# Kernel tuning notes

Measured on AMD Instinct MI355X. Metric: run time of the kernel, lower is better.

Reference implementation:

```python
import jax, jax.numpy as jnp
import numpy as np

N_NODES = 100000
N_EDGES = 3200000
N_GRAPHS = 64
NEG_SLOPE = 0.2


def mish(x):
    return x * jnp.tanh(jax.nn.softplus(x))


def gat_layer(x, src, dst, W, b, a_src, a_dst, heads, out_ch, n_nodes):
    # h: [N, H, C]
    h = (x @ W).reshape(n_nodes, heads, out_ch)
    alpha_s = jnp.sum(h * a_src[None], axis=-1)  # [N, H]
    alpha_d = jnp.sum(h * a_dst[None], axis=-1)  # [N, H]
    e = jax.nn.leaky_relu(alpha_s[src] + alpha_d[dst], NEG_SLOPE)  # [E, H]
    # scatter-softmax over incoming edges of each destination node
    emax = jax.ops.segment_max(e, dst, num_segments=n_nodes)  # [N, H]
    ee = jnp.exp(e - emax[dst])
    den = jax.ops.segment_sum(ee, dst, num_segments=n_nodes)
    alpha = ee / (den[dst] + 1e-16)  # [E, H]
    msg = h[src] * alpha[..., None]  # [E, H, C]
    out = jax.ops.segment_sum(msg, dst, num_segments=n_nodes)
    return out.reshape(n_nodes, heads * out_ch) + b


def setup_inputs() -> dict:
    key = jax.random.key(0)
    ks = jax.random.split(key, 10)
    x = jax.random.normal(ks[0], (N_NODES, 128), dtype=jnp.float32)
    edge_index = jax.random.randint(ks[1], (2, N_EDGES), 0, N_NODES, dtype=jnp.int64)
    batch = jnp.sort(jax.random.randint(ks[2], (N_NODES,), 0, N_GRAPHS, dtype=jnp.int64))
    s1 = 1.0 / np.sqrt(128.0)
    s2 = 1.0 / np.sqrt(16.0)
    return {
        "x": x,
        "edge_index": edge_index,
        "batch": batch,
        "W1": jax.random.normal(ks[3], (128, 16), dtype=jnp.float32) * s1,
        "b1": jnp.zeros((16,), dtype=jnp.float32),
        "a_src1": jax.random.normal(ks[4], (4, 4), dtype=jnp.float32) * 0.5,
        "a_dst1": jax.random.normal(ks[5], (4, 4), dtype=jnp.float32) * 0.5,
        "W2": jax.random.normal(ks[6], (16, 32), dtype=jnp.float32) * s2,
        "b2": jnp.zeros((32,), dtype=jnp.float32),
        "a_src2": jax.random.normal(ks[7], (1, 32), dtype=jnp.float32) * 0.5,
        "a_dst2": jax.random.normal(ks[8], (1, 32), dtype=jnp.float32) * 0.5,
    }


def reference(x, edge_index, batch, W1, b1, a_src1, a_dst1, W2, b2, a_src2, a_dst2):
    n = x.shape[0]
    # PyG GATConv default add_self_loops=True
    loop = jnp.arange(n, dtype=edge_index.dtype)
    src = jnp.concatenate([edge_index[0], loop])
    dst = jnp.concatenate([edge_index[1], loop])
    h = mish(gat_layer(x, src, dst, W1, b1, a_src1, a_dst1, heads=4, out_ch=4, n_nodes=n))
    h = mish(gat_layer(h, src, dst, W2, b2, a_src2, a_dst2, heads=1, out_ch=32, n_nodes=n))
    # global_mean_pool
    sums = jax.ops.segment_sum(h, batch, num_segments=N_GRAPHS)
    cnts = jax.ops.segment_sum(jnp.ones((n,), h.dtype), batch, num_segments=N_GRAPHS)
    return sums / jnp.maximum(cnts, 1.0)[:, None]
```

## Files before the change

### kernel.cpp

```cpp
#include <hip/hip_runtime.h>
#include <hip/hip_fp16.h>
#include <math.h>

#define NEG_SLOPE 0.2f
#define SB 256
#define NBMAX 1024
#define CAP 5120

typedef _Float16 half2v __attribute__((ext_vector_type(2)));

__device__ __forceinline__ float mishf(float x) {
    if (x > 15.f) return x;
    float ex = __expf(x);
    float y = 1.f + ex;
    float y2 = y * y;
    return x * (y2 - 1.f) / (y2 + 1.f);
}

__device__ __forceinline__ float lw(float e) {
    return __expf(fmaxf(e, NEG_SLOPE * e));
}

__device__ __forceinline__ float hdot2(half2v a, half2v b) {
#if __has_builtin(__builtin_amdgcn_fdot2)
    return __builtin_amdgcn_fdot2(a, b, 0.f, false);
#else
    return (float)a.x * (float)b.x + (float)a.y * (float)b.y;
#endif
}

__global__ void gemm1_kernel(const float* __restrict__ x, const float* __restrict__ W1,
                             const float* __restrict__ a_dst,
                             const float* __restrict__ W2, const float* __restrict__ as2,
                             const float* __restrict__ ad2,
                             _Float16* __restrict__ hpre1h, float* __restrict__ addst,
                             int* __restrict__ cursor, float* __restrict__ pool,
                             float* __restrict__ cnt, float* __restrict__ vs,
                             float* __restrict__ vd, int NB, int NG, int N) {
    __shared__ float Wl[128 * 16];
    __shared__ float xs[16 * 132];
    int tid = threadIdx.x;
    if (blockIdx.x == 0) {
        for (int i = tid; i < NB; i += 256) cursor[i] = 0;
        for (int i = tid; i < NG * 32; i += 256) pool[i] = 0.f;
        for (int i = tid; i < NG; i += 256) cnt[i] = 0.f;
        if (tid < 16) {
            float ps = 0.f, pd = 0.f;
            #pragma unroll
            for (int c = 0; c < 32; c++) {
                float w = W2[tid * 32 + c];
                ps += w * as2[c];
                pd += w * ad2[c];
            }
            vs[tid] = ps; vd[tid] = pd;
        }
    }
    for (int i = tid; i < 2048; i += 256) Wl[i] = W1[i];
    int nodebase = blockIdx.x * 16;
    const float4* x4 = (const float4*)(x + (size_t)nodebase * 128);
    for (int i = tid; i < 512; i += 256) {
        float4 v = x4[i];
        int e = i * 4;
        int nl = e >> 7, k = e & 127;
        float* dp = &xs[nl * 132 + k];
        dp[0] = v.x; dp[1] = v.y; dp[2] = v.z; dp[3] = v.w;
    }
    __syncthreads();
    int nl = tid >> 4, ch = tid & 15;
    const float* xr = &xs[nl * 132];
    float acc = 0.f;
    #pragma unroll 8
    for (int k = 0; k < 128; k++) acc += xr[k] * Wl[k * 16 + ch];
    int node = nodebase + nl;
    if (node < N) {
        hpre1h[node * 16 + ch] = (_Float16)acc;
        float pd = acc * a_dst[ch];
        pd += __shfl_xor(pd, 1); pd += __shfl_xor(pd, 2);
        if ((ch & 3) == 0) addst[node * 4 + (ch >> 2)] = pd;
    }
}

__global__ __launch_bounds__(1024) void scatF_kernel(
        const int* __restrict__ src, const int* __restrict__ dst,
        int E, int Etot, int CH, int NB,
        int* __restrict__ cursor, int* __restrict__ pairs) {
    __shared__ int lcnt[NBMAX];
    __shared__ int lbase[NBMAX];
    int tid = threadIdx.x, blk = blockIdx.x;
    for (int b = tid; b < NB; b += 1024) lcnt[b] = 0;
    __syncthreads();
    int ibeg = blk * CH, iend = min((blk + 1) * CH, Etot);
    for (int i = ibeg + tid; i < iend; i += 1024) {
        int d = (i < E) ? dst[i] : (i - E);
        atomicAdd(&lcnt[d >> 7], 1);
    }
    __syncthreads();
    for (int b = tid; b < NB; b += 1024) {
        int h = lcnt[b];
        lbase[b] = h ? atomicAdd(&cursor[b], h) : 0;
    }
    __syncthreads();
    for (int b = tid; b < NB; b += 1024) lcnt[b] = 0;
    __syncthreads();
    for (int i = ibeg + tid; i < iend; i += 1024) {
        int s, d;
        if (i < E) { s = src[i]; d = dst[i]; } else { s = d = i - E; }
        int b = d >> 7, dl = d & 127;
        int r = atomicAdd(&lcnt[b], 1);
        int pos = lbase[b] + r;
        pairs[(size_t)b * CAP + (pos < CAP ? pos : CAP - 1)] = s | (dl << 17);
    }
}

__global__ __launch_bounds__(512) void csragg1_kernel(
        const int* __restrict__ pairs, const int* __restrict__ btotal,
        int NB, int N,
        int* __restrict__ ssorted, int* __restrict__ rs, int* __restrict__ re,
        const float* __restrict__ a_src1, const float* __restrict__ addst,
        const _Float16* __restrict__ hpre1h, const float* __restrict__ b1,
        const float* __restrict__ vs, const float* __restrict__ vd,
        _Float16* __restrict__ hpost1h,
        float* __restrict__ as2n, float* __restrict__ ad2n) {
    __shared__ int deg[128];
    __shared__ int s[128];
    __shared__ int cur[128];
    __shared__ __attribute__((aligned(16))) int lds_sorted[CAP];
    int tid = threadIdx.x, b = blockIdx.x;
    int nb0 = b << 7;
    int cnt_nodes = min(128, N - nb0);
    int bstart = b * CAP;
    int total = min(btotal[b], CAP);
    int bend = bstart + total;
    if (tid < 128) deg[tid] = 0;
    __syncthreads();
    for (int j = bstart + tid; j < bend; j += 512)
        atomicAdd(&deg[(pairs[j] >> 17) & 127], 1);
    __syncthreads();
    if (tid < 128) s[tid] = deg[tid];
    __syncthreads();
    for (int o = 1; o < 128; o <<= 1) {
        int v = 0;
        if (tid < 128 && tid >= o) v = s[tid - o];
        __syncthreads();
        if (tid < 128) s[tid] += v;
        __syncthreads();
    }
    if (tid < 128) {
        int ex = s[tid] - deg[tid];
        cur[tid] = ex;
        if (tid < cnt_nodes) {
            rs[nb0 + tid] = bstart + ex;
            re[nb0 + tid] = bstart + ex + deg[tid];
        }
    }
    __syncthreads();
    for (int j = bstart + tid; j < bend; j += 512) {
        int p = pairs[j];
        int pos = atomicAdd(&cur[(p >> 17) & 127], 1);
        lds_sorted[pos] = p & 0x1FFFF;
    }
    __syncthreads();

    {
        int t4 = total >> 2;
        const int4* ls4 = (const int4*)lds_sorted;
        int4* gs4 = (int4*)(ssorted + bstart);
        for (int j = tid; j < t4; j += 512) gs4[j] = ls4[j];
        for (int j = (t4 << 2) + tid; j < total; j += 512)
            ssorted[bstart + j] = lds_sorted[j];
    }

    int wave = tid >> 6;
    int lane = tid & 63;
    int er = lane >> 3, hc = lane & 7, head = hc >> 1;
    int c0 = hc * 2;
    half2v wsh;
    wsh.x = (_Float16)a_src1[c0];
    wsh.y = (_Float16)a_src1[c0 + 1];
    const _Float16* hb = hpre1h + c0;
    for (int r = 0; r < 16; r++) {
        int ln = (wave << 4) + r;
        if (ln >= cnt_nodes) break;
        int node = nb0 + ln;
        int end = cur[ln];
        int start = end - deg[ln];
        float adh = addst[node * 4 + head];
        float den = 0.f, a0 = 0.f, a1 = 0.f;
        int last = end - 1;
        int jb = start;
        for (; jb + 16 <= end; jb += 16) {
            int j0 = jb + er, j1 = j0 + 8;
            int s0 = lds_sorted[j0];
            int s1 = lds_sorted[j1];
            half2v h0 = *(const half2v*)(hb + s0 * 16);
            half2v h1 = *(const half2v*)(hb + s1 * 16);
            float p0 = hdot2(h0, wsh);
            float p1 = hdot2(h1, wsh);
            float w0 = lw(p0 + __shfl_xor(p0, 1) + adh);
            float w1 = lw(p1 + __shfl_xor(p1, 1) + adh);
            den += w0 + w1;
            a0 += (float)h0.x * w0 + (float)h1.x * w1;
            a1 += (float)h0.y * w0 + (float)h1.y * w1;
        }
        if (jb < end) {
            int j0 = jb + er, j1 = j0 + 8;
            int k0 = (j0 <= last) ? j0 : last;
            int k1 = (j1 <= last) ? j1 : last;
            int s0 = lds_sorted[k0];
            int s1 = lds_sorted[k1];
            half2v h0 = *(const half2v*)(hb + s0 * 16);
            half2v h1 = *(const half2v*)(hb + s1 * 16);
            float p0 = hdot2(h0, wsh);
            float p1 = hdot2(h1, wsh);
            float e0 = p0 + __shfl_xor(p0, 1) + adh;
            float e1 = p1 + __shfl_xor(p1, 1) + adh;
            float w0 = (j0 <= last) ? lw(e0) : 0.f;
            float w1 = (j1 <= last) ? lw(e1) : 0.f;
            den += w0 + w1;
            a0 += (float)h0.x * w0 + (float)h1.x * w1;
            a1 += (float)h0.y * w0 + (float)h1.y * w1;
        }
        a0 += __shfl_xor(a0, 8);  a1 += __shfl_xor(a1, 8);  den += __shfl_xor(den, 8);
        a0 += __shfl_xor(a0, 16); a1 += __shfl_xor(a1, 16); den += __shfl_xor(den, 16);
        a0 += __shfl_xor(a0, 32); a1 += __shfl_xor(a1, 32); den += __shfl_xor(den, 32);
        if (er == 0) {
            float inv = 1.f / (den + 1e-16f);
            float o0 = mishf(a0 * inv + b1[c0]);
            float o1 = mishf(a1 * inv + b1[c0 + 1]);
            half2v oh;
            oh.x = (_Float16)o0; oh.y = (_Float16)o1;
            *(half2v*)(hpost1h + node * 16 + c0) = oh;
            float ps = o0 * vs[c0] + o1 * vs[c0 + 1];
            float pd = o0 * vd[c0] + o1 * vd[c0 + 1];
            ps += __shfl_xor(ps, 1); pd += __shfl_xor(pd, 1);
            ps += __shfl_xor(ps, 2); pd += __shfl_xor(pd, 2);
            ps += __shfl_xor(ps, 4); pd += __shfl_xor(pd, 4);
            if (hc == 0) { as2n[node] = ps; ad2n[node] = pd; }
        }
    }
}

__global__ void agg2_kernel(const int* __restrict__ rs, const int* __restrict__ re,
                            const int* __restrict__ ssorted,
                            const float* __restrict__ as2n, const float* __restrict__ ad2n,
                            const _Float16* __restrict__ hpost1h,
                            float* __restrict__ agg16, float* __restrict__ denv, int N) {
    int wave = threadIdx.x >> 6;
    int lane = threadIdx.x & 63;
    int node = blockIdx.x * 4 + wave;
    if (node >= N) return;
    int start = rs[node], end = re[node];
    int er = lane >> 3, hc = lane & 7;
    int c0 = hc * 2;
    float adh = ad2n[node];
    const _Float16* hb = hpost1h + c0;
    float den = 0.f, a0 = 0.f, a1 = 0.f;
    int last = end - 1;
    int jb = start;
    for (; jb + 16 <= end; jb += 16) {
        int j0 = jb + er, j1 = j0 + 8;
        int s0 = __builtin_nontemporal_load(ssorted + j0);
        int s1 = __builtin_nontemporal_load(ssorted + j1);
        float e0 = as2n[s0] + adh;
        float e1 = as2n[s1] + adh;
        half2v h0 = *(const half2v*)(hb + s0 * 16);
        half2v h1 = *(const half2v*)(hb + s1 * 16);
        float w0 = lw(e0);
        float w1 = lw(e1);
        den += w0 + w1;
        a0 += (float)h0.x * w0 + (float)h1.x * w1;
        a1 += (float)h0.y * w0 + (float)h1.y * w1;
    }
    if (jb < end) {
        int j0 = jb + er, j1 = j0 + 8;
        int k0 = (j0 <= last) ? j0 : last;
        int k1 = (j1 <= last) ? j1 : last;
        int s0 = __builtin_nontemporal_load(ssorted + k0);
        int s1 = __builtin_nontemporal_load(ssorted + k1);
        float e0 = as2n[s0] + adh;
        float e1 = as2n[s1] + adh;
        half2v h0 = *(const half2v*)(hb + s0 * 16);
        half2v h1 = *(const half2v*)(hb + s1 * 16);
        float w0 = (j0 <= last) ? lw(e0) : 0.f;
        float w1 = (j1 <= last) ? lw(e1) : 0.f;
        den += w0 + w1;
        a0 += (float)h0.x * w0 + (float)h1.x * w1;
        a1 += (float)h0.y * w0 + (float)h1.y * w1;
    }
    a0 += __shfl_xor(a0, 8);  a1 += __shfl_xor(a1, 8);  den += __shfl_xor(den, 8);
    a0 += __shfl_xor(a0, 16); a1 += __shfl_xor(a1, 16); den += __shfl_xor(den, 16);
    a0 += __shfl_xor(a0, 32); a1 += __shfl_xor(a1, 32); den += __shfl_xor(den, 32);
    if (er == 0) {
        float2 o; o.x = a0; o.y = a1;
        *(float2*)(agg16 + node * 16 + c0) = o;
        if (hc == 0) denv[node] = den;
    }
}

__global__ void post2pool_kernel(const float* __restrict__ agg16, const float* __restrict__ denv,
                                 const float* __restrict__ W2, const float* __restrict__ b2,
                                 const int* __restrict__ batch,
                                 float* __restrict__ pool, float* __restrict__ cnt, int N) {
    __shared__ float Wl[16 * 32];
    int tid = threadIdx.x;
    for (int i = tid; i < 512; i += 256) Wl[i] = W2[i];
    __syncthreads();
    int r = tid >> 5, ch = tid & 31;
    float bc = b2[ch];
    int base = blockIdx.x * 512;
    int cur = -1;
    float sum = 0.f, c = 0.f;
    for (int it = 0; it < 64; it++) {
        int n = base + it * 8 + r;
        if (n >= N) break;
        int g = batch[n];
        if (g != cur) {
            if (cur >= 0) {
                atomicAdd(&pool[cur * 32 + ch], sum);
                if (ch == 0) atomicAdd(&cnt[cur], c);
            }
            cur = g; sum = 0.f; c = 0.f;
        }
        const float* ar = agg16 + (size_t)n * 16;
        float acc = 0.f;
        #pragma unroll
        for (int k = 0; k < 16; k++) acc += ar[k] * Wl[k * 32 + ch];
        float val = mishf(acc / (denv[n] + 1e-16f) + bc);
        sum += val;
        c += 1.f;
    }
    if (cur >= 0) {
        atomicAdd(&pool[cur * 32 + ch], sum);
        if (ch == 0) atomicAdd(&cnt[cur], c);
    }
}

__global__ void fin_kernel(const float* __restrict__ pool, const float* __restrict__ cnt,
                           float* __restrict__ out, int NG) {
    int i = blockIdx.x * blockDim.x + threadIdx.x;
    if (i >= NG * 32) return;
    out[i] = pool[i] / fmaxf(cnt[i >> 5], 1.0f);
}

extern "C" void kernel_launch(void* const* d_in, const int* in_sizes, int n_in,
                              void* d_out, int out_size, void* d_ws, size_t ws_size,
                              hipStream_t stream) {
    const float* x   = (const float*)d_in[0];
    const int* eidx  = (const int*)d_in[1];
    const int* batch = (const int*)d_in[2];
    const float* W1  = (const float*)d_in[3];
    const float* b1  = (const float*)d_in[4];
    const float* as1 = (const float*)d_in[5];
    const float* ad1 = (const float*)d_in[6];
    const float* W2  = (const float*)d_in[7];
    const float* b2  = (const float*)d_in[8];
    const float* as2 = (const float*)d_in[9];
    const float* ad2 = (const float*)d_in[10];
    float* out = (float*)d_out;

    int N = in_sizes[0] / 128;
    int E = in_sizes[1] / 2;
    int Etot = E + N;
    int NG = out_size / 32;
    const int* esrc = eidx;
    const int* edst = eidx + E;

    int NB = (N + 127) >> 7;
    int CH = (Etot + SB - 1) / SB;

    char* p = (char*)d_ws;
    auto alloc = [&](size_t nbytes) {
        p = (char*)(((uintptr_t)p + 15) & ~(uintptr_t)15);
        void* r = (void*)p; p += nbytes; return r;
    };
    int* pairs        = (int*)alloc((size_t)NB * CAP * 4);
    int* ssorted      = (int*)alloc((size_t)NB * CAP * 4);
    int* rs           = (int*)alloc((size_t)N * 4);
    int* re           = (int*)alloc((size_t)N * 4);
    int* cursor       = (int*)alloc((size_t)NB * 4);
    _Float16* hpre1h  = (_Float16*)alloc((size_t)N * 16 * 2);
    _Float16* hpost1h = (_Float16*)alloc((size_t)N * 16 * 2);
    float* addst1  = (float*)alloc((size_t)N * 4 * 4);
    float* as2n    = (float*)alloc((size_t)N * 4);
    float* ad2n    = (float*)alloc((size_t)N * 4);
    float* agg16   = (float*)alloc((size_t)N * 16 * 4);
    float* denv    = (float*)alloc((size_t)N * 4);
    float* vs      = (float*)alloc(16 * 4);
    float* vd      = (float*)alloc(16 * 4);
    float* pool    = (float*)alloc((size_t)NG * 32 * 4);
    float* cnt     = (float*)alloc((size_t)NG * 4);

    gemm1_kernel<<<(N + 15) / 16, 256, 0, stream>>>(x, W1, ad1, W2, as2, ad2,
                                                    hpre1h, addst1, cursor, pool, cnt,
                                                    vs, vd, NB, NG, N);
    scatF_kernel<<<SB, 1024, 0, stream>>>(esrc, edst, E, Etot, CH, NB, cursor, pairs);
    csragg1_kernel<<<NB, 512, 0, stream>>>(pairs, cursor, NB, N,
                                           ssorted, rs, re, as1, addst1, hpre1h,
                                           b1, vs, vd, hpost1h, as2n, ad2n);
    agg2_kernel<<<(N + 3) / 4, 256, 0, stream>>>(rs, re, ssorted, as2n, ad2n, hpost1h,
                                                 agg16, denv, N);
    post2pool_kernel<<<(N + 511) / 512, 256, 0, stream>>>(agg16, denv, W2, b2, batch,
                                                          pool, cnt, N);
    fin_kernel<<<(NG * 32 + 255) / 256, 256, 0, stream>>>(pool, cnt, out, NG);
}
```

Before: 330.6 us.

## Halve destination buckets, widen per-lane gathers to 4 halves, vectorize GEMM1 and scatter

Destination buckets shrink from 128 to 64 nodes, so there are twice as many blocks in scatter and csragg1, each with less LDS. The gather lanes in both aggregation kernels now load 4 halves (one full head) per edge instead of 2, which removes the cross-lane shuffle for the attention dot product. GEMM1 transposes W into LDS so the inner loop can read float4. The scatter kernel caches dst indices in registers so they are not reloaded in the second pass. Risks include bucket overflow at CAP 2816 (clamped writes would corrupt results for high-degree buckets) and higher register pressure.

```diff
diff --git a/kernel.cpp b/kernel.cpp
--- a/kernel.cpp
+++ b/kernel.cpp
@@ -3,11 +3,12 @@
 #include <math.h>
 
 #define NEG_SLOPE 0.2f
-#define SB 256
-#define NBMAX 1024
-#define CAP 5120
+#define SB 512
+#define NBMAX 2048
+#define CAP 2816
 
 typedef _Float16 half2v __attribute__((ext_vector_type(2)));
+typedef _Float16 half4v __attribute__((ext_vector_type(4)));
 
 __device__ __forceinline__ float mishf(float x) {
     if (x > 15.f) return x;
@@ -21,11 +22,11 @@
     return __expf(fmaxf(e, NEG_SLOPE * e));
 }
 
-__device__ __forceinline__ float hdot2(half2v a, half2v b) {
+__device__ __forceinline__ float hdot2a(half2v a, half2v b, float c) {
 #if __has_builtin(__builtin_amdgcn_fdot2)
-    return __builtin_amdgcn_fdot2(a, b, 0.f, false);
+    return __builtin_amdgcn_fdot2(a, b, c, false);
 #else
-    return (float)a.x * (float)b.x + (float)a.y * (float)b.y;
+    return (float)a.x * (float)b.x + (float)a.y * (float)b.y + c;
 #endif
 }
 
@@ -37,7 +38,7 @@
                              int* __restrict__ cursor, float* __restrict__ pool,
                              float* __restrict__ cnt, float* __restrict__ vs,
                              float* __restrict__ vd, int NB, int NG, int N) {
-    __shared__ float Wl[128 * 16];
+    __shared__ float Wlt[16 * 132];
     __shared__ float xs[16 * 132];
     int tid = threadIdx.x;
     if (blockIdx.x == 0) {
@@ -55,7 +56,7 @@
             vs[tid] = ps; vd[tid] = pd;
         }
     }
-    for (int i = tid; i < 2048; i += 256) Wl[i] = W1[i];
+    for (int i = tid; i < 2048; i += 256) Wlt[(i & 15) * 132 + (i >> 4)] = W1[i];
     int nodebase = blockIdx.x * 16;
     const float4* x4 = (const float4*)(x + (size_t)nodebase * 128);
     for (int i = tid; i < 512; i += 256) {
@@ -67,10 +68,15 @@
     }
     __syncthreads();
     int nl = tid >> 4, ch = tid & 15;
-    const float* xr = &xs[nl * 132];
+    const float4* xr4 = (const float4*)&xs[nl * 132];
+    const float4* wr4 = (const float4*)&Wlt[ch * 132];
     float acc = 0.f;
-    #pragma unroll 8
-    for (int k = 0; k < 128; k++) acc += xr[k] * Wl[k * 16 + ch];
+    #pragma unroll
+    for (int k4 = 0; k4 < 32; k4++) {
+        float4 xv = xr4[k4];
+        float4 wv = wr4[k4];
+        acc += xv.x * wv.x + xv.y * wv.y + xv.z * wv.z + xv.w * wv.w;
+    }
     int node = nodebase + nl;
     if (node < N) {
         hpre1h[node * 16 + ch] = (_Float16)acc;
@@ -90,9 +96,18 @@
     for (int b = tid; b < NB; b += 1024) lcnt[b] = 0;
     __syncthreads();
     int ibeg = blk * CH, iend = min((blk + 1) * CH, Etot);
-    for (int i = ibeg + tid; i < iend; i += 1024) {
+    int cd[8];
+    #pragma unroll
+    for (int u = 0; u < 8; u++) {
+        int i = ibeg + tid + (u << 10);
+        int d = -1;
+        if (i < iend) d = (i < E) ? dst[i] : (i - E);
+        cd[u] = d;
+        if (d >= 0) atomicAdd(&lcnt[d >> 6], 1);
+    }
+    for (int i = ibeg + (8 << 10) + tid; i < iend; i += 1024) {
         int d = (i < E) ? dst[i] : (i - E);
-        atomicAdd(&lcnt[d >> 7], 1);
+        atomicAdd(&lcnt[d >> 6], 1);
     }
     __syncthreads();
     for (int b = tid; b < NB; b += 1024) {
@@ -102,17 +117,28 @@
     __syncthreads();
     for (int b = tid; b < NB; b += 1024) lcnt[b] = 0;
     __syncthreads();
-    for (int i = ibeg + tid; i < iend; i += 1024) {
-        int s, d;
-        if (i < E) { s = src[i]; d = dst[i]; } else { s = d = i - E; }
-        int b = d >> 7, dl = d & 127;
+    #pragma unroll
+    for (int u = 0; u < 8; u++) {
+        int i = ibeg + tid + (u << 10);
+        int d = cd[u];
+        if (d < 0) continue;
+        int s = (i < E) ? src[i] : d;
+        int b = d >> 6, dl = d & 63;
         int r = atomicAdd(&lcnt[b], 1);
         int pos = lbase[b] + r;
         pairs[(size_t)b * CAP + (pos < CAP ? pos : CAP - 1)] = s | (dl << 17);
     }
-}
-
-__global__ __launch_bounds__(512) void csragg1_kernel(
+    for (int i = ibeg + (8 << 10) + tid; i < iend; i += 1024) {
+        int d = (i < E) ? dst[i] : (i - E);
+        int s = (i < E) ? src[i] : d;
+        int b = d >> 6, dl = d & 63;
+        int r = atomicAdd(&lcnt[b], 1);
+        int pos = lbase[b] + r;
+        pairs[(size_t)b * CAP + (pos < CAP ? pos : CAP - 1)] = s | (dl << 17);
+    }
+}
+
+__global__ __launch_bounds__(256) void csragg1_kernel(
         const int* __restrict__ pairs, const int* __restrict__ btotal,
         int NB, int N,
         int* __restrict__ ssorted, int* __restrict__ rs, int* __restrict__ re,
@@ -121,31 +147,31 @@
         const float* __restrict__ vs, const float* __restrict__ vd,
         _Float16* __restrict__ hpost1h,
         float* __restrict__ as2n, float* __restrict__ ad2n) {
-    __shared__ int deg[128];
-    __shared__ int s[128];
-    __shared__ int cur[128];
+    __shared__ int deg[64];
+    __shared__ int s[64];
+    __shared__ int cur[64];
     __shared__ __attribute__((aligned(16))) int lds_sorted[CAP];
     int tid = threadIdx.x, b = blockIdx.x;
-    int nb0 = b << 7;
-    int cnt_nodes = min(128, N - nb0);
+    int nb0 = b << 6;
+    int cnt_nodes = min(64, N - nb0);
     int bstart = b * CAP;
     int total = min(btotal[b], CAP);
     int bend = bstart + total;
-    if (tid < 128) deg[tid] = 0;
-    __syncthreads();
-    for (int j = bstart + tid; j < bend; j += 512)
-        atomicAdd(&deg[(pairs[j] >> 17) & 127], 1);
-    __syncthreads();
-    if (tid < 128) s[tid] = deg[tid];
-    __syncthreads();
-    for (int o = 1; o < 128; o <<= 1) {
+    if (tid < 64) deg[tid] = 0;
+    __syncthreads();
+    for (int j = bstart + tid; j < bend; j += 256)
+        atomicAdd(&deg[(pairs[j] >> 17) & 63], 1);
+    __syncthreads();
+    if (tid < 64) s[tid] = deg[tid];
+    __syncthreads();
+    for (int o = 1; o < 64; o <<= 1) {
         int v = 0;
-        if (tid < 128 && tid >= o) v = s[tid - o];
+        if (tid < 64 && tid >= o) v = s[tid - o];
         __syncthreads();
-        if (tid < 128) s[tid] += v;
+        if (tid < 64) s[tid] += v;
         __syncthreads();
     }
-    if (tid < 128) {
+    if (tid < 64) {
         int ex = s[tid] - deg[tid];
         cur[tid] = ex;
         if (tid < cnt_nodes) {
@@ -154,9 +180,9 @@
         }
     }
     __syncthreads();
-    for (int j = bstart + tid; j < bend; j += 512) {
+    for (int j = bstart + tid; j < bend; j += 256) {
         int p = pairs[j];
-        int pos = atomicAdd(&cur[(p >> 17) & 127], 1);
+        int pos = atomicAdd(&cur[(p >> 17) & 63], 1);
         lds_sorted[pos] = p & 0x1FFFF;
     }
     __syncthreads();
@@ -165,19 +191,18 @@
         int t4 = total >> 2;
         const int4* ls4 = (const int4*)lds_sorted;
         int4* gs4 = (int4*)(ssorted + bstart);
-        for (int j = tid; j < t4; j += 512) gs4[j] = ls4[j];
-        for (int j = (t4 << 2) + tid; j < total; j += 512)
+        for (int j = tid; j < t4; j += 256) gs4[j] = ls4[j];
+        for (int j = (t4 << 2) + tid; j < total; j += 256)
             ssorted[bstart + j] = lds_sorted[j];
     }
 
     int wave = tid >> 6;
     int lane = tid & 63;
-    int er = lane >> 3, hc = lane & 7, head = hc >> 1;
-    int c0 = hc * 2;
-    half2v wsh;
-    wsh.x = (_Float16)a_src1[c0];
-    wsh.y = (_Float16)a_src1[c0 + 1];
-    const _Float16* hb = hpre1h + c0;
+    int head = lane & 3, er = lane >> 2;
+    int c0 = head * 4;
+    half2v w01, w23;
+    w01.x = (_Float16)a_src1[c0];     w01.y = (_Float16)a_src1[c0 + 1];
+    w23.x = (_Float16)a_src1[c0 + 2]; w23.y = (_Float16)a_src1[c0 + 3];
     for (int r = 0; r < 16; r++) {
         int ln = (wave << 4) + r;
         if (ln >= cnt_nodes) break;
@@ -185,57 +210,52 @@
         int end = cur[ln];
         int start = end - deg[ln];
         float adh = addst[node * 4 + head];
-        float den = 0.f, a0 = 0.f, a1 = 0.f;
+        float den = 0.f, a0 = 0.f, a1 = 0.f, a2 = 0.f, a3 = 0.f;
         int last = end - 1;
         int jb = start;
         for (; jb + 16 <= end; jb += 16) {
-            int j0 = jb + er, j1 = j0 + 8;
-            int s0 = lds_sorted[j0];
-            int s1 = lds_sorted[j1];
-            half2v h0 = *(const half2v*)(hb + s0 * 16);
-            half2v h1 = *(const half2v*)(hb + s1 * 16);
-            float p0 = hdot2(h0, wsh);
-            float p1 = hdot2(h1, wsh);
-            float w0 = lw(p0 + __shfl_xor(p0, 1) + adh);
-            float w1 = lw(p1 + __shfl_xor(p1, 1) + adh);
-            den += w0 + w1;
-            a0 += (float)h0.x * w0 + (float)h1.x * w1;
-            a1 += (float)h0.y * w0 + (float)h1.y * w1;
+            int s0 = lds_sorted[jb + er];
+            half4v h = *(const half4v*)(hpre1h + (size_t)s0 * 16 + c0);
+            half2v hlo = __builtin_shufflevector(h, h, 0, 1);
+            half2v hhi = __builtin_shufflevector(h, h, 2, 3);
+            float p = hdot2a(hlo, w01, hdot2a(hhi, w23, 0.f));
+            float w = lw(p + adh);
+            den += w;
+            a0 += (float)h.x * w; a1 += (float)h.y * w;
+            a2 += (float)h.z * w; a3 += (float)h.w * w;
         }
         if (jb < end) {
-            int j0 = jb + er, j1 = j0 + 8;
+            int j0 = jb + er;
             int k0 = (j0 <= last) ? j0 : last;
-            int k1 = (j1 <= last) ? j1 : last;
             int s0 = lds_sorted[k0];
-            int s1 = lds_sorted[k1];
-            half2v h0 = *(const half2v*)(hb + s0 * 16);
-            half2v h1 = *(const half2v*)(hb + s1 * 16);
-            float p0 = hdot2(h0, wsh);
-            float p1 = hdot2(h1, wsh);
-            float e0 = p0 + __shfl_xor(p0, 1) + adh;
-            float e1 = p1 + __shfl_xor(p1, 1) + adh;
-            float w0 = (j0 <= last) ? lw(e0) : 0.f;
-            float w1 = (j1 <= last) ? lw(e1) : 0.f;
-            den += w0 + w1;
-            a0 += (float)h0.x * w0 + (float)h1.x * w1;
-            a1 += (float)h0.y * w0 + (float)h1.y * w1;
-        }
-        a0 += __shfl_xor(a0, 8);  a1 += __shfl_xor(a1, 8);  den += __shfl_xor(den, 8);
-        a0 += __shfl_xor(a0, 16); a1 += __shfl_xor(a1, 16); den += __shfl_xor(den, 16);
-        a0 += __shfl_xor(a0, 32); a1 += __shfl_xor(a1, 32); den += __shfl_xor(den, 32);
+            half4v h = *(const half4v*)(hpre1h + (size_t)s0 * 16 + c0);
+            half2v hlo = __builtin_shufflevector(h, h, 0, 1);
+            half2v hhi = __builtin_shufflevector(h, h, 2, 3);
+            float p = hdot2a(hlo, w01, hdot2a(hhi, w23, 0.f));
+            float w = (j0 <= last) ? lw(p + adh) : 0.f;
+            den += w;
+            a0 += (float)h.x * w; a1 += (float)h.y * w;
+            a2 += (float)h.z * w; a3 += (float)h.w * w;
+        }
+        a0 += __shfl_xor(a0, 4);  a1 += __shfl_xor(a1, 4);  a2 += __shfl_xor(a2, 4);  a3 += __shfl_xor(a3, 4);  den += __shfl_xor(den, 4);
+        a0 += __shfl_xor(a0, 8);  a1 += __shfl_xor(a1, 8);  a2 += __shfl_xor(a2, 8);  a3 += __shfl_xor(a3, 8);  den += __shfl_xor(den, 8);
+        a0 += __shfl_xor(a0, 16); a1 += __shfl_xor(a1, 16); a2 += __shfl_xor(a2, 16); a3 += __shfl_xor(a3, 16); den += __shfl_xor(den, 16);
+        a0 += __shfl_xor(a0, 32); a1 += __shfl_xor(a1, 32); a2 += __shfl_xor(a2, 32); a3 += __shfl_xor(a3, 32); den += __shfl_xor(den, 32);
         if (er == 0) {
             float inv = 1.f / (den + 1e-16f);
             float o0 = mishf(a0 * inv + b1[c0]);
             float o1 = mishf(a1 * inv + b1[c0 + 1]);
-            half2v oh;
+            float o2 = mishf(a2 * inv + b1[c0 + 2]);
+            float o3 = mishf(a3 * inv + b1[c0 + 3]);
+            half4v oh;
             oh.x = (_Float16)o0; oh.y = (_Float16)o1;
-            *(half2v*)(hpost1h + node * 16 + c0) = oh;
-            float ps = o0 * vs[c0] + o1 * vs[c0 + 1];
-            float pd = o0 * vd[c0] + o1 * vd[c0 + 1];
+            oh.z = (_Float16)o2; oh.w = (_Float16)o3;
+            *(half4v*)(hpost1h + (size_t)node * 16 + c0) = oh;
+            float ps = o0 * vs[c0] + o1 * vs[c0 + 1] + o2 * vs[c0 + 2] + o3 * vs[c0 + 3];
+            float pd = o0 * vd[c0] + o1 * vd[c0 + 1] + o2 * vd[c0 + 2] + o3 * vd[c0 + 3];
             ps += __shfl_xor(ps, 1); pd += __shfl_xor(pd, 1);
             ps += __shfl_xor(ps, 2); pd += __shfl_xor(pd, 2);
-            ps += __shfl_xor(ps, 4); pd += __shfl_xor(pd, 4);
-            if (hc == 0) { as2n[node] = ps; ad2n[node] = pd; }
+            if (head == 0) { as2n[node] = ps; ad2n[node] = pd; }
         }
     }
 }
@@ -250,50 +270,39 @@
     int node = blockIdx.x * 4 + wave;
     if (node >= N) return;
     int start = rs[node], end = re[node];
-    int er = lane >> 3, hc = lane & 7;
-    int c0 = hc * 2;
+    int q = lane & 3, er = lane >> 2;
+    int c0 = q * 4;
     float adh = ad2n[node];
     const _Float16* hb = hpost1h + c0;
-    float den = 0.f, a0 = 0.f, a1 = 0.f;
+    float den = 0.f, a0 = 0.f, a1 = 0.f, a2 = 0.f, a3 = 0.f;
     int last = end - 1;
     int jb = start;
     for (; jb + 16 <= end; jb += 16) {
-        int j0 = jb + er, j1 = j0 + 8;
-        int s0 = __builtin_nontemporal_load(ssorted + j0);
-        int s1 = __builtin_nontemporal_load(ssorted + j1);
-        float e0 = as2n[s0] + adh;
-        float e1 = as2n[s1] + adh;
-        half2v h0 = *(const half2v*)(hb + s0 * 16);
-        half2v h1 = *(const half2v*)(hb + s1 * 16);
-        float w0 = lw(e0);
-        float w1 = lw(e1);
-        den += w0 + w1;
-        a0 += (float)h0.x * w0 + (float)h1.x * w1;
-        a1 += (float)h0.y * w0 + (float)h1.y * w1;
+        int s0 = __builtin_nontemporal_load(ssorted + jb + er);
+        float w = lw(as2n[s0] + adh);
+        half4v h = *(const half4v*)(hb + (size_t)s0 * 16);
+        den += w;
+        a0 += (float)h.x * w; a1 += (float)h.y * w;
+        a2 += (float)h.z * w; a3 += (float)h.w * w;
     }
     if (jb < end) {
-        int j0 = jb + er, j1 = j0 + 8;
+        int j0 = jb + er;
         int k0 = (j0 <= last) ? j0 : last;
-        int k1 = (j1 <= last) ? j1 : last;
         int s0 = __builtin_nontemporal_load(ssorted + k0);
-        int s1 = __builtin_nontemporal_load(ssorted + k1);
-        float e0 = as2n[s0] + adh;
-        float e1 = as2n[s1] + adh;
-        half2v h0 = *(const half2v*)(hb + s0 * 16);
-        half2v h1 = *(const half2v*)(hb + s1 * 16);
-        float w0 = (j0 <= last) ? lw(e0) : 0.f;
-        float w1 = (j1 <= last) ? lw(e1) : 0.f;
-        den += w0 + w1;
-        a0 += (float)h0.x * w0 + (float)h1.x * w1;
-        a1 += (float)h0.y * w0 + (float)h1.y * w1;
-    }
-    a0 += __shfl_xor(a0, 8);  a1 += __shfl_xor(a1, 8);  den += __shfl_xor(den, 8);
-    a0 += __shfl_xor(a0, 16); a1 += __shfl_xor(a1, 16); den += __shfl_xor(den, 16);
-    a0 += __shfl_xor(a0, 32); a1 += __shfl_xor(a1, 32); den += __shfl_xor(den, 32);
+        float w = (j0 <= last) ? lw(as2n[s0] + adh) : 0.f;
+        half4v h = *(const half4v*)(hb + (size_t)s0 * 16);
+        den += w;
+        a0 += (float)h.x * w; a1 += (float)h.y * w;
+        a2 += (float)h.z * w; a3 += (float)h.w * w;
+    }
+    a0 += __shfl_xor(a0, 4);  a1 += __shfl_xor(a1, 4);  a2 += __shfl_xor(a2, 4);  a3 += __shfl_xor(a3, 4);  den += __shfl_xor(den, 4);
+    a0 += __shfl_xor(a0, 8);  a1 += __shfl_xor(a1, 8);  a2 += __shfl_xor(a2, 8);  a3 += __shfl_xor(a3, 8);  den += __shfl_xor(den, 8);
+    a0 += __shfl_xor(a0, 16); a1 += __shfl_xor(a1, 16); a2 += __shfl_xor(a2, 16); a3 += __shfl_xor(a3, 16); den += __shfl_xor(den, 16);
+    a0 += __shfl_xor(a0, 32); a1 += __shfl_xor(a1, 32); a2 += __shfl_xor(a2, 32); a3 += __shfl_xor(a3, 32); den += __shfl_xor(den, 32);
     if (er == 0) {
-        float2 o; o.x = a0; o.y = a1;
-        *(float2*)(agg16 + node * 16 + c0) = o;
-        if (hc == 0) denv[node] = den;
+        float4 o; o.x = a0; o.y = a1; o.z = a2; o.w = a3;
+        *(float4*)(agg16 + (size_t)node * 16 + c0) = o;
+        if (q == 0) denv[node] = den;
     }
 }
 
@@ -365,7 +374,7 @@
     const int* esrc = eidx;
     const int* edst = eidx + E;
 
-    int NB = (N + 127) >> 7;
+    int NB = (N + 63) >> 6;
     int CH = (Etot + SB - 1) / SB;
 
     char* p = (char*)d_ws;
@@ -394,7 +403,7 @@
                                                     hpre1h, addst1, cursor, pool, cnt,
                                                     vs, vd, NB, NG, N);
     scatF_kernel<<<SB, 1024, 0, stream>>>(esrc, edst, E, Etot, CH, NB, cursor, pairs);
-    csragg1_kernel<<<NB, 512, 0, stream>>>(pairs, cursor, NB, N,
+    csragg1_kernel<<<NB, 256, 0, stream>>>(pairs, cursor, NB, N,
                                            ssorted, rs, re, as1, addst1, hpre1h,
                                            b1, vs, vd, hpost1h, as2n, ad2n);
     agg2_kernel<<<(N + 3) / 4, 256, 0, stream>>>(rs, re, ssorted, as2n, ad2n, hpost1h,
```

New measurement: 336.1 us. No clear change (+1.7%).
